# Kernel tuning notes

Measured on AMD Instinct MI355X. Metric: run time of the kernel, lower is better.

The kernel has to match this reference:

```python
import jax, jax.numpy as jnp
import numpy as np
import math

B, S, DIM = 2, 4096, 1024
H, HD = 16, 64            # n_heads, head_dim
BLK, TOPK = 512, 3        # moba_block_size, moba_topk
NEG_INF = -10000.0


def setup_inputs() -> dict:
    key = jax.random.key(0)
    ks = jax.random.split(key, 5)
    scale = 1.0 / math.sqrt(DIM)
    x = jax.random.normal(ks[0], (B, S, DIM), dtype=jnp.float32)
    wq = jax.random.normal(ks[1], (DIM, DIM), dtype=jnp.float32) * scale
    wk = jax.random.normal(ks[2], (DIM, DIM), dtype=jnp.float32) * scale
    wv = jax.random.normal(ks[3], (DIM, DIM), dtype=jnp.float32) * scale
    wo = jax.random.normal(ks[4], (DIM, DIM), dtype=jnp.float32) * scale
    # rotary tables over half of head_dim
    inv_freq = 1.0 / (10000.0 ** (jnp.arange(0, HD, 2, dtype=jnp.float32) / HD))
    ang = jnp.arange(S, dtype=jnp.float32)[:, None] * inv_freq[None, :]  # [S, HD//2]
    return {"x": x, "wq": wq, "wk": wk, "wv": wv, "wo": wo,
            "cos": jnp.cos(ang), "sin": jnp.sin(ang)}


def _rotate(t, cos, sin):
    # t: [B, H, S, HD]; rotate-half rotary embedding
    c = cos[None, None, :, :]
    s = sin[None, None, :, :]
    t1, t2 = jnp.split(t, 2, axis=-1)
    return jnp.concatenate([t1 * c - t2 * s, t1 * s + t2 * c], axis=-1)


def _moba_forward(x, wq, wk, wv, wo, cos, sin):
    bs, seq_len, dim = x.shape
    inv_sqrt_d = 1.0 / math.sqrt(HD)
    q = (x @ wq).reshape(bs, seq_len, H, HD).transpose(0, 2, 1, 3)  # [B,H,S,D]
    k = (x @ wk).reshape(bs, seq_len, H, HD).transpose(0, 2, 1, 3)
    v = (x @ wv).reshape(bs, seq_len, H, HD).transpose(0, 2, 1, 3)
    q = _rotate(q, cos, sin)
    k = _rotate(k, cos, sin)

    nb = seq_len // BLK  # num_blocks (S divisible by BLK -> pad_len = 0)
    k_blocks = k.reshape(bs, H, nb, BLK, HD)
    v_blocks = v.reshape(bs, H, nb, BLK, HD)

    # gating: q against block means, with block-causal mask
    block_repr = k_blocks.mean(axis=3)  # [B,H,nb,D]
    gating = jnp.einsum('bhsd,bhnd->bhsn', q, block_repr) * inv_sqrt_d
    q_block = jnp.arange(seq_len) // BLK
    future = q_block[:, None] < jnp.arange(nb)[None, :]  # [S, nb]
    gating = jnp.where(future[None, None], NEG_INF, gating)
    _, sel = jax.lax.top_k(gating, TOPK)  # [B,H,S,TOPK]

    # one chunk per block of queries; chunk uses indices of its middle query
    nc = seq_len // BLK
    mids = jnp.arange(nc) * BLK + BLK // 2
    chunk_sel = sel[:, :, mids, :]  # [B,H,nc,TOPK]

    idx = chunk_sel.reshape(bs, H, nc * TOPK)[..., None, None]  # [B,H,nc*k,1,1]
    k_sel = jnp.take_along_axis(k_blocks, idx, axis=2).reshape(bs, H, nc, TOPK * BLK, HD)
    v_sel = jnp.take_along_axis(v_blocks, idx, axis=2).reshape(bs, H, nc, TOPK * BLK, HD)

    q_ch = q.reshape(bs, H, nc, BLK, HD)
    scores = jnp.einsum('bhcqd,bhckd->bhcqk', q_ch, k_sel) * inv_sqrt_d
    probs = jax.nn.softmax(scores.astype(jnp.float32), axis=-1).astype(scores.dtype)
    out = jnp.einsum('bhcqk,bhckd->bhcqd', probs, v_sel)  # [B,H,nc,BLK,D]
    out = out.reshape(bs, H, seq_len, HD).transpose(0, 2, 1, 3).reshape(bs, seq_len, dim)
    return out @ wo


def reference(x, wq, wk, wv, wo, cos, sin):
    return _moba_forward(x, wq, wk, wv, wo, cos, sin)
```

## Files before the change

### kernel.cpp

```cpp
#include <hip/hip_runtime.h>

typedef short bf16x8 __attribute__((ext_vector_type(8)));
typedef float f32x4 __attribute__((ext_vector_type(4)));
typedef float f32x16 __attribute__((ext_vector_type(16)));

#define AS1 __attribute__((address_space(1)))
#define AS3 __attribute__((address_space(3)))
#define GLOAD16(g, l) __builtin_amdgcn_global_load_lds((const AS1 unsigned int*)(g), (AS3 unsigned int*)(l), 16, 0, 0)

#define B_   2
#define S_   4096
#define DIM_ 1024
#define H_   16
#define HD_  64
#define BLK_ 512
#define SCLQ 0.18033688011112042f

static __device__ __forceinline__ unsigned short f2bf(float x){
  unsigned int u = __builtin_bit_cast(unsigned int, x);
  u += 0x7fffu + ((u >> 16) & 1u);
  return (unsigned short)(u >> 16);
}

static __device__ __forceinline__ unsigned cvtpk(float lo, float hi){
  unsigned r;
  asm("v_cvt_pk_bf16_f32 %0, %1, %2" : "=v"(r) : "v"(lo), "v"(hi));
  return r;
}
static __device__ __forceinline__ void plswap(unsigned &a, unsigned &b){
  asm("v_permlane32_swap_b32 %0, %1" : "+v"(a), "+v"(b));
}
static __device__ __forceinline__ bf16x8 mkpa(unsigned a, unsigned b, unsigned c, unsigned d){
  int4 v = make_int4((int)a,(int)b,(int)c,(int)d);
  return __builtin_bit_cast(bf16x8, v);
}

__global__ __launch_bounds__(256) void k_convert_x(const float4* __restrict__ x, ushort4* __restrict__ xb){
  int i = blockIdx.x * 256 + threadIdx.x;
  float4 v = x[i];
  xb[i] = make_ushort4(f2bf(v.x), f2bf(v.y), f2bf(v.z), f2bf(v.w));
}

__global__ __launch_bounds__(256) void k_transpose_w(
    const float* __restrict__ w0, const float* __restrict__ w1,
    const float* __restrict__ w2, const float* __restrict__ w3,
    unsigned short* __restrict__ wqkvT, unsigned short* __restrict__ woT){
  __shared__ float tl[32][33];
  int z = blockIdx.z;
  const float* w = z==0 ? w0 : z==1 ? w1 : z==2 ? w2 : w3;
  unsigned short* t = (z==3) ? woT : (wqkvT + (size_t)z*1024*1024);
  int nb = blockIdx.x*32, kb = blockIdx.y*32;
  int tx = threadIdx.x & 31, ty = threadIdx.x >> 5;
  #pragma unroll
  for(int i=0;i<4;i++) tl[ty+8*i][tx] = w[(size_t)(kb+ty+8*i)*DIM_ + nb+tx];
  __syncthreads();
  #pragma unroll
  for(int i=0;i<4;i++) t[(size_t)(nb+ty+8*i)*DIM_ + kb+tx] = f2bf(tl[tx][ty+8*i]);
}

__global__ __launch_bounds__(256) void k_xp(const float* __restrict__ x,
                                            const float* __restrict__ cosT, const float* __restrict__ sinT,
                                            float* __restrict__ Xp2){
  __shared__ float Xl[16*128];
  __shared__ float Wl[16*64];
  int bid = blockIdx.x;
  int dt = bid & 7, ss = (bid>>3)&1, n = (bid>>4)&7, b = bid>>7;
  int tid = threadIdx.x;
  int jt = tid & 15, dtl = tid >> 4;
  int dbase = dt*128;
  int s0 = n*512 + ss*256;
  f32x4 acc[8];
  #pragma unroll
  for(int i=0;i<8;i++) acc[i] = (f32x4){0.f,0.f,0.f,0.f};

  for(int ch=0; ch<16; ch++){
    int sb = s0 + ch*16;
    #pragma unroll
    for(int i=0;i<2;i++){
      int g = i*256 + tid;
      int row = g>>5, col = g&31;
      GLOAD16(x + ((size_t)b*S_ + sb + row)*DIM_ + dbase + col*4, (char*)Xl + g*16);
    }
    {
      int row = tid>>4, col = tid&15;
      const float* src = (col < 8) ? (cosT + (size_t)(sb + row)*32 + col*4)
                                   : (sinT + (size_t)(sb + row)*32 + (col-8)*4);
      GLOAD16(src, (char*)Wl + tid*16);
    }
    __syncthreads();
    #pragma unroll
    for(int s=0;s<16;s++){
      f32x4 wv = *(const f32x4*)&Wl[s*64 + jt*4];
      f32x4 x0 = *(const f32x4*)&Xl[s*128 + dtl*8];
      f32x4 x1 = *(const f32x4*)&Xl[s*128 + dtl*8 + 4];
      #pragma unroll
      for(int dd=0;dd<4;dd++) acc[dd]   += wv * x0[dd];
      #pragma unroll
      for(int dd=0;dd<4;dd++) acc[dd+4] += wv * x1[dd];
    }
    __syncthreads();
  }
  size_t base = ((size_t)(ss*16 + b*8 + n))*1024;
  #pragma unroll
  for(int dd=0;dd<8;dd++){
    size_t row = base + dbase + dtl*8 + dd;
    *(f32x4*)&Xp2[row*64 + jt*4] = acc[dd];
  }
}

__global__ __launch_bounds__(256) void k_bsum(const float* __restrict__ Xp2, const float* __restrict__ wk,
                                              float* __restrict__ bsum){
  __shared__ float red[4][64];
  int bid = blockIdx.x;
  int h = bid & 15, n = (bid>>4)&7, b = bid>>7;
  int tid = threadIdx.x;
  int jj = tid & 63, dgrp = tid >> 6;
  int j = jj & 31;
  size_t r0 = ((size_t)(b*8 + n))*1024;
  size_t r1 = ((size_t)(16 + b*8 + n))*1024;
  float acc = 0.0f;
  for(int i=0;i<256;i++){
    int d = dgrp*256 + i;
    float xc = Xp2[(r0 + d)*64 + j]      + Xp2[(r1 + d)*64 + j];
    float xs = Xp2[(r0 + d)*64 + 32 + j] + Xp2[(r1 + d)*64 + 32 + j];
    float u = wk[(size_t)d*1024 + h*64 + j];
    float v = wk[(size_t)d*1024 + h*64 + 32 + j];
    acc += (jj < 32) ? (xc*u - xs*v) : (xs*u + xc*v);
  }
  red[dgrp][jj] = acc;
  __syncthreads();
  if(tid < 64){
    float s = red[0][tid] + red[1][tid] + red[2][tid] + red[3][tid];
    bsum[(((size_t)(b*16+h))*8 + n)*64 + tid] = s;
  }
}

__global__ __launch_bounds__(256) void k_qmid(const float* __restrict__ x, const float* __restrict__ wq,
                                              float* __restrict__ qpart){
  __shared__ float xr[128];
  int bid = blockIdx.x;
  int ks  = blockIdx.y;
  int b = bid >> 3, c = bid & 7;
  int mid = c*BLK_ + BLK_/2;
  int tid = threadIdx.x;
  if(tid < 128) xr[tid] = x[((size_t)b*S_ + mid)*DIM_ + ks*128 + tid];
  __syncthreads();
  float acc[4] = {0,0,0,0};
  for(int k=0;k<128;k++){
    float xv = xr[k];
    #pragma unroll
    for(int i=0;i<4;i++) acc[i] += xv * wq[(size_t)(ks*128+k)*1024 + i*256 + tid];
  }
  #pragma unroll
  for(int i=0;i<4;i++) qpart[((size_t)ks*16 + bid)*1024 + i*256 + tid] = acc[i];
}

__global__ __launch_bounds__(256) void k_sel(const float* __restrict__ qpart, const float* __restrict__ bsum,
                                             const float* __restrict__ cosT, const float* __restrict__ sinT,
                                             int* __restrict__ sel){
  int bid = blockIdx.x;
  int b = bid >> 3, c = bid & 7;
  int mid = c*BLK_ + BLK_/2;
  int tid = threadIdx.x;
  int hg = tid >> 4, ln = tid & 15;
  size_t qb0 = (size_t)bid*1024 + hg*64;
  auto qsum = [&](int idx){
    float s = 0.0f;
    #pragma unroll
    for(int ks=0;ks<8;ks++) s += qpart[(size_t)ks*16384 + qb0 + idx];
    return s;
  };
  float rv[4];
  #pragma unroll
  for(int i=0;i<4;i++){
    int jj = ln*4 + i; int j = jj & 31;
    float q1 = qsum(j), q2 = qsum(32+j);
    float c0 = cosT[(size_t)mid*32 + j], s0 = sinT[(size_t)mid*32 + j];
    rv[i] = (jj < 32) ? (q1*c0 - q2*s0) : (q1*s0 + q2*c0);
  }
  float g[8];
  #pragma unroll
  for(int n=0;n<8;n++){
    const float* bs = bsum + (((size_t)(b*16+hg))*8 + n)*64 + ln*4;
    float p = rv[0]*bs[0] + rv[1]*bs[1] + rv[2]*bs[2] + rv[3]*bs[3];
    p += __shfl_xor(p,1); p += __shfl_xor(p,2); p += __shfl_xor(p,4); p += __shfl_xor(p,8);
    g[n] = p * (1.0f/512.0f) * 0.125f;
  }
  if(ln == 0){
    for(int n=c+1;n<8;n++) g[n] = -10000.0f;
    int base = ((b*16+hg)*8 + c)*3;
    #pragma unroll
    for(int t=0;t<3;t++){
      int bi = 0; float bv = g[0];
      for(int n=1;n<8;n++) if(g[n] > bv){ bv = g[n]; bi = n; }
      sel[base + t] = bi;
      g[bi] = -3.4e38f;
    }
  }
}

template<int MODE>
__global__ __launch_bounds__(512, 2) void k_gemmq(const unsigned short* __restrict__ A,
                                                  const unsigned short* __restrict__ Bt,
                                                  unsigned short* __restrict__ dq, unsigned short* __restrict__ dk,
                                                  unsigned short* __restrict__ dv, float* __restrict__ dstf,
                                                  const float* __restrict__ cosT, const float* __restrict__ sinT,
                                                  int M, int N, int K, int NBN){
  __shared__ unsigned short lA[2][128*64];
  __shared__ unsigned short lB[2][128*64];
  int nwg = gridDim.x;
  int chunk = nwg >> 3;
  int id = blockIdx.x;
  int swz = (id & 7)*chunk + (id >> 3);
  int bm = (swz / NBN)*128, bn = (swz % NBN)*128;
  int tid = threadIdx.x, w = tid>>6, lane = tid&63;
  int wr = w>>1, wc = w&1;
  int l15 = lane&15, lh = lane>>4;
  f32x4 acc[2][4];
  f32x4 zero = {0.f,0.f,0.f,0.f};
  #pragma unroll
  for(int m=0;m<2;m++)
    #pragma unroll
    for(int n=0;n<4;n++) acc[m][n] = zero;

  auto STAGE = [&](int bsel, int k0){
    #pragma unroll
    for(int i=0;i<2;i++){
      int g = i*512 + tid;
      int row = g>>3, slot = (g&7)^(row&7);
      GLOAD16(A  + (size_t)(bm+row)*K + k0 + slot*8, (char*)lA[bsel] + g*16);
      GLOAD16(Bt + (size_t)(bn+row)*K + k0 + slot*8, (char*)lB[bsel] + g*16);
    }
  };

  int NT = K >> 6;
  STAGE(0, 0);
  STAGE(1, 64);
  int cur = 0;

  for(int t=0;t<NT;t++){
    if(t < NT-1) asm volatile("s_waitcnt vmcnt(4)" ::: "memory");
    else         asm volatile("s_waitcnt vmcnt(0)" ::: "memory");
    asm volatile("s_barrier" ::: "memory");

    #pragma unroll
    for(int kk=0;kk<2;kk++){
      bf16x8 af[2], bfr[4];
      #pragma unroll
      for(int m=0;m<2;m++){
        int r = wr*32 + m*16 + l15;
        af[m] = *(const bf16x8*)((const char*)lA[cur] + r*128 + (((kk*4+lh)^(r&7))*16));
      }
      #pragma unroll
      for(int n=0;n<4;n++){
        int r = wc*64 + n*16 + l15;
        bfr[n] = *(const bf16x8*)((const char*)lB[cur] + r*128 + (((kk*4+lh)^(r&7))*16));
      }
      __builtin_amdgcn_s_setprio(1);
      #pragma unroll
      for(int m=0;m<2;m++)
        #pragma unroll
        for(int n=0;n<4;n++)
          acc[m][n] = __builtin_amdgcn_mfma_f32_16x16x32_bf16(af[m], bfr[n], acc[m][n], 0, 0, 0);
      __builtin_amdgcn_s_setprio(0);
    }

    asm volatile("s_barrier" ::: "memory");
    if(t+2 < NT) STAGE(cur, (t+2)*64);
    cur ^= 1;
  }

  if(MODE == 2){
    #pragma unroll
    for(int m=0;m<2;m++){
      int row0 = bm + wr*32 + m*16 + lh*4;
      #pragma unroll
      for(int n=0;n<4;n++){
        int col = bn + wc*64 + n*16 + l15;
        #pragma unroll
        for(int r=0;r<4;r++) dstf[(size_t)(row0+r)*N + col] = acc[m][n][r];
      }
    }
  } else {
    int sec = bn >> 10;
    int nloc = (bn & 1023) + wc*64;
    if(sec == 2){
      #pragma unroll
      for(int m=0;m<2;m++){
        int s0 = bm + wr*32 + m*16 + lh*4;
        int bb = s0 >> 12, sl = s0 & 4095;
        #pragma unroll
        for(int n=0;n<4;n++){
          int d = nloc + n*16 + l15;
          ushort4 pk = make_ushort4(f2bf(acc[m][n][0]), f2bf(acc[m][n][1]),
                                    f2bf(acc[m][n][2]), f2bf(acc[m][n][3]));
          *(ushort4*)&dv[((size_t)(bb*1024 + d))*4096 + sl] = pk;
        }
      }
    } else {
      unsigned short* dst = (sec == 0) ? dq : dk;
      float scl = (sec == 0) ? SCLQ : 1.0f;
      int h = nloc >> 6;
      #pragma unroll
      for(int m=0;m<2;m++){
        int row0 = bm + wr*32 + m*16 + lh*4;
        #pragma unroll
        for(int n=0;n<2;n++){
          int f = n*16 + l15;
          #pragma unroll
          for(int r=0;r<4;r++){
            int row = row0 + r;
            int bb = row >> 12, s = row & 4095;
            float c0 = cosT[(size_t)s*32 + f]*scl, s0 = sinT[(size_t)s*32 + f]*scl;
            float a1 = acc[m][n][r], a2 = acc[m][n+2][r];
            size_t base = ((size_t)(bb*16 + h)*4096 + s)*64;
            dst[base + f]      = f2bf(a1*c0 - a2*s0);
            dst[base + 32 + f] = f2bf(a1*s0 + a2*c0);
          }
        }
      }
    }
  }
}

__global__ __launch_bounds__(256, 4) void k_attn(const unsigned short* __restrict__ q,
                                                 const unsigned short* __restrict__ kb,
                                                 const unsigned short* __restrict__ vt,
                                                 const int* __restrict__ sel,
                                                 unsigned short* __restrict__ attnb){
  __shared__ unsigned short lK[2][64*64];
  __shared__ unsigned short lV[2][64*64];
  int cbh = blockIdx.x, qt = blockIdx.y;
  int bh = cbh >> 3, c = cbh & 7;
  int b = bh >> 4, h = bh & 15;
  int tid = threadIdx.x, w = tid>>6, lane = tid&63;
  int ql = lane&31, hi = lane>>5;
  int q0 = c*BLK_ + qt*128 + w*32;

  const int* selp = sel + (bh*8 + c)*3;
  int sb0 = selp[0], sb1 = selp[1], sb2 = selp[2];

  int r0 = tid>>3, sl = (tid&7) ^ (r0&7);
  const unsigned short* kbase = kb + ((size_t)bh*S_ + r0)*64 + (size_t)sl*8;
  const unsigned short* vbase = vt + ((size_t)(b*1024 + h*64 + r0))*S_ + (size_t)sl*8;

  bf16x8 qf[4];
  #pragma unroll
  for(int kk=0;kk<4;kk++)
    qf[kk] = *(const bf16x8*)(q + ((size_t)bh*S_ + q0 + ql)*64 + kk*16 + hi*8);

  f32x16 o[2], o2;
  f32x16 zero16 = {0,0,0,0,0,0,0,0,0,0,0,0,0,0,0,0};
  o[0] = zero16; o[1] = zero16; o2 = zero16;
  short one_bf = (short)0x3F80;
  bf16x8 ones = {one_bf,one_bf,one_bf,one_bf,one_bf,one_bf,one_bf,one_bf};

  auto STAGE = [&](int bsel, int t){
    int seg = t>>3;
    int blk = seg==0 ? sb0 : (seg==1 ? sb1 : sb2);
    int soff = blk*BLK_ + (t&7)*64;
    #pragma unroll
    for(int i=0;i<2;i++){
      GLOAD16(kbase + (size_t)(soff + i*32)*64, (char*)lK[bsel] + (i*256 + w*64)*16);
      GLOAD16(vbase + (size_t)i*32*S_ + soff,   (char*)lV[bsel] + (i*256 + w*64)*16);
    }
  };

  STAGE(0, 0);
  __syncthreads();
  int cur = 0;

  for(int t=0;t<24;t++){
    if(t+1 < 24) STAGE(cur^1, t+1);

    f32x16 sc[2];
    sc[0] = zero16; sc[1] = zero16;
    __builtin_amdgcn_s_setprio(1);
    #pragma unroll
    for(int g=0;g<2;g++){
      int key = g*32 + ql;
      #pragma unroll
      for(int kk=0;kk<4;kk++){
        bf16x8 kf = *(const bf16x8*)((const char*)lK[cur] + key*128 + ((kk*32 + hi*16) ^ ((ql&7)<<4)));
        sc[g] = __builtin_amdgcn_mfma_f32_32x32x16_bf16(kf, qf[kk], sc[g], 0, 0, 0);
      }
    }
    __builtin_amdgcn_s_setprio(0);

    #pragma unroll
    for(int r=0;r<16;r++){
      sc[0][r] = exp2f(sc[0][r]);
      sc[1][r] = exp2f(sc[1][r]);
    }

    __builtin_amdgcn_s_setprio(1);
    #pragma unroll
    for(int g=0;g<2;g++){
      unsigned u0 = cvtpk(sc[g][0],  sc[g][1]);
      unsigned u1 = cvtpk(sc[g][4],  sc[g][5]);
      plswap(u0, u1);
      unsigned u2 = cvtpk(sc[g][2],  sc[g][3]);
      unsigned u3 = cvtpk(sc[g][6],  sc[g][7]);
      plswap(u2, u3);
      unsigned u4 = cvtpk(sc[g][8],  sc[g][9]);
      unsigned u5 = cvtpk(sc[g][12], sc[g][13]);
      plswap(u4, u5);
      unsigned u6 = cvtpk(sc[g][10], sc[g][11]);
      unsigned u7 = cvtpk(sc[g][14], sc[g][15]);
      plswap(u6, u7);
      bf16x8 pa0 = mkpa(u0,u2,u1,u3);
      bf16x8 pa1 = mkpa(u4,u6,u5,u7);
      #pragma unroll
      for(int dh=0;dh<2;dh++){
        int d = dh*32 + ql;
        bf16x8 v0 = *(const bf16x8*)((const char*)lV[cur] + d*128 + ((g*64 + hi*16) ^ ((d&7)<<4)));
        o[dh] = __builtin_amdgcn_mfma_f32_32x32x16_bf16(pa0, v0, o[dh], 0, 0, 0);
        bf16x8 v1 = *(const bf16x8*)((const char*)lV[cur] + d*128 + ((g*64 + 32 + hi*16) ^ ((d&7)<<4)));
        o[dh] = __builtin_amdgcn_mfma_f32_32x32x16_bf16(pa1, v1, o[dh], 0, 0, 0);
      }
      o2 = __builtin_amdgcn_mfma_f32_32x32x16_bf16(pa0, ones, o2, 0, 0, 0);
      o2 = __builtin_amdgcn_mfma_f32_32x32x16_bf16(pa1, ones, o2, 0, 0, 0);
    }
    __builtin_amdgcn_s_setprio(0);

    __syncthreads();
    cur ^= 1;
  }

  #pragma unroll
  for(int r=0;r<16;r++){
    float inv = 1.0f / o2[r];
    int cr = (r&3) + 8*(r>>2) + 4*hi;
    int s = q0 + cr;
    size_t base = ((size_t)(b*S_ + s))*1024 + h*64;
    attnb[base + ql]      = f2bf(o[0][r]*inv);
    attnb[base + 32 + ql] = f2bf(o[1][r]*inv);
  }
}

extern "C" void kernel_launch(void* const* d_in, const int* in_sizes, int n_in,
                              void* d_out, int out_size, void* d_ws, size_t ws_size,
                              hipStream_t stream){
  const float* x    = (const float*)d_in[0];
  const float* wq   = (const float*)d_in[1];
  const float* wk   = (const float*)d_in[2];
  const float* wv   = (const float*)d_in[3];
  const float* wo   = (const float*)d_in[4];
  const float* cosT = (const float*)d_in[5];
  const float* sinT = (const float*)d_in[6];

  char* p = (char*)d_ws;
  unsigned short* xbf   = (unsigned short*)p; p += (size_t)8192*1024*2;
  unsigned short* wqkvT = (unsigned short*)p; p += (size_t)3072*1024*2;
  unsigned short* woT   = (unsigned short*)p; p += (size_t)1024*1024*2;
  unsigned short* qb  = (unsigned short*)p; p += (size_t)8192*1024*2;
  unsigned short* kbf = (unsigned short*)p; p += (size_t)8192*1024*2;
  unsigned short* vtb = (unsigned short*)p; p += (size_t)8192*1024*2;
  float* qpart = (float*)p; p += (size_t)8*16*1024*4;
  float* Xp2  = (float*)p; p += (size_t)2*16*1024*64*4;
  float* bsum = (float*)p; p += (size_t)2*16*8*64*4;
  int*   sel  = (int*)p;   p += (size_t)2*16*8*3*4;
  unsigned short* attnb = xbf;
  if((size_t)(p - (char*)d_ws) > ws_size) return;

  k_convert_x<<<8192, 256, 0, stream>>>((const float4*)x, (ushort4*)xbf);
  k_transpose_w<<<dim3(32,32,4), 256, 0, stream>>>(wq,wk,wv,wo, wqkvT, woT);
  k_xp<<<256, 256, 0, stream>>>(x, cosT, sinT, Xp2);
  k_bsum<<<256, 256, 0, stream>>>(Xp2, wk, bsum);
  k_qmid<<<dim3(16,8), 256, 0, stream>>>(x, wq, qpart);
  k_sel<<<16, 256, 0, stream>>>(qpart, bsum, cosT, sinT, sel);
  k_gemmq<0><<<1536, 512, 0, stream>>>(xbf, wqkvT, qb, kbf, vtb, nullptr, cosT, sinT, 8192, 3072, 1024, 24);
  k_attn<<<dim3(256,4), 256, 0, stream>>>(qb, kbf, vtb, sel, attnb);
  k_gemmq<2><<<512, 512, 0, stream>>>(attnb, woT, nullptr, nullptr, nullptr, (float*)d_out, nullptr, nullptr, 8192, 1024, 1024, 8);
}
```

Measured before the change: 266.6 us.

## Use 256x128 tiles with triple-buffered LDS for the fused QKV GEMM

The QKV projection GEMM moves from the shared template kernel into a dedicated kernel. It uses 256x128 output tiles (4x4 MFMA fragments per wave) and a three-stage global-to-LDS pipeline, with vmcnt waits tuned to that depth, and the grid is halved to 768 blocks. The larger tile is meant to raise arithmetic intensity and data reuse per LDS load, and the deeper pipeline to hide load latency. The cost is about 147 KB of LDS per block, which likely allows only one block per CU despite the launch bound, plus more accumulator registers. The output projection keeps the old 128x128 kernel, now without the template mode switch.

```diff
diff --git a/kernel.cpp b/kernel.cpp
--- a/kernel.cpp
+++ b/kernel.cpp
@@ -199,12 +199,124 @@
   }
 }
 
-template<int MODE>
-__global__ __launch_bounds__(512, 2) void k_gemmq(const unsigned short* __restrict__ A,
+__global__ __launch_bounds__(512, 2) void k_gemmw(const unsigned short* __restrict__ A,
                                                   const unsigned short* __restrict__ Bt,
                                                   unsigned short* __restrict__ dq, unsigned short* __restrict__ dk,
-                                                  unsigned short* __restrict__ dv, float* __restrict__ dstf,
-                                                  const float* __restrict__ cosT, const float* __restrict__ sinT,
+                                                  unsigned short* __restrict__ dv,
+                                                  const float* __restrict__ cosT, const float* __restrict__ sinT){
+  const int K = 1024;
+  __shared__ unsigned short lA[3][256*64];
+  __shared__ unsigned short lB[3][128*64];
+  int id = blockIdx.x;
+  int swz = (id & 7)*96 + (id >> 3);
+  int bm = (swz / 24)*256, bn = (swz % 24)*128;
+  int tid = threadIdx.x, w = tid>>6, lane = tid&63;
+  int wr = w>>1, wc = w&1;
+  int l15 = lane&15, lh = lane>>4;
+  f32x4 acc[4][4];
+  f32x4 zero = {0.f,0.f,0.f,0.f};
+  #pragma unroll
+  for(int m=0;m<4;m++)
+    #pragma unroll
+    for(int n=0;n<4;n++) acc[m][n] = zero;
+
+  auto STAGE = [&](int bsel, int k0){
+    #pragma unroll
+    for(int i=0;i<4;i++){
+      int g = i*512 + tid;
+      int row = g>>3, slot = (g&7)^(row&7);
+      GLOAD16(A + (size_t)(bm+row)*K + k0 + slot*8, (char*)lA[bsel] + g*16);
+    }
+    #pragma unroll
+    for(int i=0;i<2;i++){
+      int g = i*512 + tid;
+      int row = g>>3, slot = (g&7)^(row&7);
+      GLOAD16(Bt + (size_t)(bn+row)*K + k0 + slot*8, (char*)lB[bsel] + g*16);
+    }
+  };
+
+  const int NT = 16;
+  STAGE(0, 0);
+  STAGE(1, 64);
+  STAGE(2, 128);
+  int cur = 0;
+
+  for(int t=0;t<NT;t++){
+    if(t < NT-2)      asm volatile("s_waitcnt vmcnt(12)" ::: "memory");
+    else if(t == NT-2) asm volatile("s_waitcnt vmcnt(6)"  ::: "memory");
+    else               asm volatile("s_waitcnt vmcnt(0)"  ::: "memory");
+    asm volatile("s_barrier" ::: "memory");
+
+    #pragma unroll
+    for(int kk=0;kk<2;kk++){
+      bf16x8 af[4], bfr[4];
+      #pragma unroll
+      for(int m=0;m<4;m++){
+        int r = wr*64 + m*16 + l15;
+        af[m] = *(const bf16x8*)((const char*)lA[cur] + r*128 + (((kk*4+lh)^(r&7))*16));
+      }
+      #pragma unroll
+      for(int n=0;n<4;n++){
+        int r = wc*64 + n*16 + l15;
+        bfr[n] = *(const bf16x8*)((const char*)lB[cur] + r*128 + (((kk*4+lh)^(r&7))*16));
+      }
+      __builtin_amdgcn_s_setprio(1);
+      #pragma unroll
+      for(int m=0;m<4;m++)
+        #pragma unroll
+        for(int n=0;n<4;n++)
+          acc[m][n] = __builtin_amdgcn_mfma_f32_16x16x32_bf16(af[m], bfr[n], acc[m][n], 0, 0, 0);
+      __builtin_amdgcn_s_setprio(0);
+    }
+
+    asm volatile("s_barrier" ::: "memory");
+    if(t+3 < NT) STAGE(cur, (t+3)*64);
+    cur = (cur==2) ? 0 : cur+1;
+  }
+
+  int sec = bn >> 10;
+  int nloc = (bn & 1023) + wc*64;
+  if(sec == 2){
+    #pragma unroll
+    for(int m=0;m<4;m++){
+      int s0 = bm + wr*64 + m*16 + lh*4;
+      int bb = s0 >> 12, sl = s0 & 4095;
+      #pragma unroll
+      for(int n=0;n<4;n++){
+        int d = nloc + n*16 + l15;
+        ushort4 pk = make_ushort4(f2bf(acc[m][n][0]), f2bf(acc[m][n][1]),
+                                  f2bf(acc[m][n][2]), f2bf(acc[m][n][3]));
+        *(ushort4*)&dv[((size_t)(bb*1024 + d))*4096 + sl] = pk;
+      }
+    }
+  } else {
+    unsigned short* dst = (sec == 0) ? dq : dk;
+    float scl = (sec == 0) ? SCLQ : 1.0f;
+    int h = nloc >> 6;
+    #pragma unroll
+    for(int m=0;m<4;m++){
+      int row0 = bm + wr*64 + m*16 + lh*4;
+      #pragma unroll
+      for(int n=0;n<2;n++){
+        int f = n*16 + l15;
+        #pragma unroll
+        for(int r=0;r<4;r++){
+          int row = row0 + r;
+          int bb = row >> 12, s = row & 4095;
+          float c0 = cosT[(size_t)s*32 + f]*scl, s0 = sinT[(size_t)s*32 + f]*scl;
+          float a1 = acc[m][n][r], a2 = acc[m][n+2][r];
+          size_t base = ((size_t)(bb*16 + h)*4096 + s)*64;
+          dst[base + f]      = f2bf(a1*c0 - a2*s0);
+          dst[base + 32 + f] = f2bf(a1*s0 + a2*c0);
+        }
+      }
+    }
+  }
+}
+
+__global__ __launch_bounds__(512, 2) void k_gemmo(const unsigned short* __restrict__ A,
+                                                  const unsigned short* __restrict__ Bt,
+                                                  float* __restrict__ dstf,
                                                   int M, int N, int K, int NBN){
   __shared__ unsigned short lA[2][128*64];
   __shared__ unsigned short lB[2][128*64];
@@ -270,55 +382,14 @@
     cur ^= 1;
   }
 
-  if(MODE == 2){
-    #pragma unroll
-    for(int m=0;m<2;m++){
-      int row0 = bm + wr*32 + m*16 + lh*4;
-      #pragma unroll
-      for(int n=0;n<4;n++){
-        int col = bn + wc*64 + n*16 + l15;
-        #pragma unroll
-        for(int r=0;r<4;r++) dstf[(size_t)(row0+r)*N + col] = acc[m][n][r];
-      }
-    }
-  } else {
-    int sec = bn >> 10;
-    int nloc = (bn & 1023) + wc*64;
-    if(sec == 2){
-      #pragma unroll
-      for(int m=0;m<2;m++){
-        int s0 = bm + wr*32 + m*16 + lh*4;
-        int bb = s0 >> 12, sl = s0 & 4095;
-        #pragma unroll
-        for(int n=0;n<4;n++){
-          int d = nloc + n*16 + l15;
-          ushort4 pk = make_ushort4(f2bf(acc[m][n][0]), f2bf(acc[m][n][1]),
-                                    f2bf(acc[m][n][2]), f2bf(acc[m][n][3]));
-          *(ushort4*)&dv[((size_t)(bb*1024 + d))*4096 + sl] = pk;
-        }
-      }
-    } else {
-      unsigned short* dst = (sec == 0) ? dq : dk;
-      float scl = (sec == 0) ? SCLQ : 1.0f;
-      int h = nloc >> 6;
-      #pragma unroll
-      for(int m=0;m<2;m++){
-        int row0 = bm + wr*32 + m*16 + lh*4;
-        #pragma unroll
-        for(int n=0;n<2;n++){
-          int f = n*16 + l15;
-          #pragma unroll
-          for(int r=0;r<4;r++){
-            int row = row0 + r;
-            int bb = row >> 12, s = row & 4095;
-            float c0 = cosT[(size_t)s*32 + f]*scl, s0 = sinT[(size_t)s*32 + f]*scl;
-            float a1 = acc[m][n][r], a2 = acc[m][n+2][r];
-            size_t base = ((size_t)(bb*16 + h)*4096 + s)*64;
-            dst[base + f]      = f2bf(a1*c0 - a2*s0);
-            dst[base + 32 + f] = f2bf(a1*s0 + a2*c0);
-          }
-        }
-      }
+  #pragma unroll
+  for(int m=0;m<2;m++){
+    int row0 = bm + wr*32 + m*16 + lh*4;
+    #pragma unroll
+    for(int n=0;n<4;n++){
+      int col = bn + wc*64 + n*16 + l15;
+      #pragma unroll
+      for(int r=0;r<4;r++) dstf[(size_t)(row0+r)*N + col] = acc[m][n][r];
     }
   }
 }
@@ -469,7 +540,7 @@
   k_bsum<<<256, 256, 0, stream>>>(Xp2, wk, bsum);
   k_qmid<<<dim3(16,8), 256, 0, stream>>>(x, wq, qpart);
   k_sel<<<16, 256, 0, stream>>>(qpart, bsum, cosT, sinT, sel);
-  k_gemmq<0><<<1536, 512, 0, stream>>>(xbf, wqkvT, qb, kbf, vtb, nullptr, cosT, sinT, 8192, 3072, 1024, 24);
+  k_gemmw<<<768, 512, 0, stream>>>(xbf, wqkvT, qb, kbf, vtb, cosT, sinT);
   k_attn<<<dim3(256,4), 256, 0, stream>>>(qb, kbf, vtb, sel, attnb);
-  k_gemmq<2><<<512, 512, 0, stream>>>(attnb, woT, nullptr, nullptr, nullptr, (float*)d_out, nullptr, nullptr, 8192, 1024, 1024, 8);
-}
+  k_gemmo<<<512, 512, 0, stream>>>(attnb, woT, (float*)d_out, 8192, 1024, 1024, 8);
+}
```

New measurement: 268.2 us. About the same (+0.6%).
